# Optimization experiments

Measured on AMD Instinct MI355X. Metric: run time of the kernel, lower is better.

## Reference

```python
import jax, jax.numpy as jnp
import numpy as np

N_QUBITS = 14
QLCU_LAYERS = 2
BATCH = 128
N_PARAMS = 5 * N_QUBITS * QLCU_LAYERS  # 140


def _rx(t):
    # RX(theta) = [[cos(t/2), -i sin(t/2)], [-i sin(t/2), cos(t/2)]], batched over B -> [B,2,2]
    c = jnp.cos(t * 0.5).astype(jnp.complex64)
    s = (-1j * jnp.sin(t * 0.5)).astype(jnp.complex64)
    return jnp.stack([jnp.stack([c, s], -1), jnp.stack([s, c], -1)], -2)


def _ry(t):
    c = jnp.cos(t * 0.5)
    s = jnp.sin(t * 0.5)
    m = jnp.stack([jnp.stack([c, -s], -1), jnp.stack([s, c], -1)], -2)
    return m.astype(jnp.complex64)


def _rz(t):
    e = jnp.exp(-0.5j * t.astype(jnp.complex64))
    z = jnp.zeros_like(e)
    return jnp.stack([jnp.stack([e, z], -1), jnp.stack([z, jnp.conj(e)], -1)], -2)


def _apply_1q(state, gate, w):
    # state: [B] + [2]*n (wire 0 = most significant axis, PennyLane convention); gate: [B,2,2]
    s = jnp.moveaxis(state, w + 1, 1)
    s = jnp.einsum('bij,bj...->bi...', gate, s)
    return jnp.moveaxis(s, 1, w + 1)


def _apply_crx(state, theta, c, t):
    # controlled-RX: apply RX(theta) on target wire t in the control==1 subspace
    gate = _rx(theta)
    st = jnp.moveaxis(state, c + 1, 1)
    s0, s1 = st[:, 0], st[:, 1]
    ta = t if t > c else t + 1  # target axis inside s1 (control axis removed)
    s1 = jnp.moveaxis(s1, ta, 1)
    s1 = jnp.einsum('bij,bj...->bi...', gate, s1)
    s1 = jnp.moveaxis(s1, 1, ta)
    st = jnp.stack([s0, s1], axis=1)
    return jnp.moveaxis(st, 1, c + 1)


def _circuit(params):
    B = params.shape[0]
    n = N_QUBITS
    state = jnp.zeros((B,) + (2,) * n, jnp.complex64)
    state = state.at[(slice(None),) + (0,) * n].set(1.0)  # |0...0>
    idx = 0
    for _ in range(QLCU_LAYERS):
        for i in range(n):
            state = _apply_1q(state, _rx(params[:, idx]), i)
            state = _apply_1q(state, _ry(params[:, idx + 1]), i)
            state = _apply_1q(state, _rz(params[:, idx + 2]), i)
            idx += 3
        for i in range(n):
            state = _apply_crx(state, params[:, idx], i, (i + 1) % n)
            idx += 1
        for i in range(n - 1, -1, -1):
            state = _apply_crx(state, params[:, idx], i, (i - 1) % n)
            idx += 1
    return state.reshape(B, 2 ** n)


def setup_inputs() -> dict:
    key = jax.random.key(0)
    params = jax.random.normal(key, (BATCH, N_PARAMS), dtype=jnp.float32)
    return {"params": params}


def reference(params):
    # Returns the batched quantum state vector [B, 2**n_qubits] (complex64),
    # matching qml.state() wire ordering (wire 0 = MSB).
    return _circuit(params)
```

## Files before the change

kernel.cpp:

```cpp
#include <hip/hip_runtime.h>
#include <math.h>

constexpr int NQ      = 14;
constexpr int NSTATE  = 1 << 14;
constexpr int NF4     = NSTATE / 2;
constexpr int NPARAMS = 140;
constexpr int BATCH   = 128;
constexpr int THREADS = 1024;

__device__ __forceinline__ unsigned int f2bf(float f) {
    union { float f; unsigned int u; } v; v.f = f;
    return (v.u + 0x7FFFu + ((v.u >> 16) & 1u)) >> 16;
}
__device__ __forceinline__ int SWZ4(int f) { return f ^ ((f >> 3) & 7); }

__device__ __forceinline__ void u_half2(float& ax, float& ay, float& bx, float& by,
                                        float ur, float ui, float vr, float vi) {
    float a0x = ax, a0y = ay, a1x = bx, a1y = by;
    ax =  ur*a0x - ui*a0y + vr*a1x - vi*a1y;
    ay =  ur*a0y + ui*a0x + vr*a1y + vi*a1x;
    bx = -vr*a0x - vi*a0y + ur*a1x + ui*a1y;
    by = -vr*a0y + vi*a0x + ur*a1y - ui*a1x;
}
__device__ __forceinline__ void crx_half(float& ax, float& ay, float& bx, float& by,
                                         float cr, float sr) {
    float a0x = ax, a0y = ay, a1x = bx, a1y = by;
    ax = cr*a0x + sr*a1y;  ay = cr*a0y - sr*a1x;
    bx = cr*a1x + sr*a0y;  by = cr*a1y - sr*a0x;
}

struct G  { int type, pb, c, t; };
struct P2 { int nb, b0, b1, b2, ng; G g0, g1, g2; };

constexpr P2 PS[18] = {
    {3,13,12,11, 3, {0,0,0,13},  {0,3,0,12},  {0,6,0,11}},
    {3,10,9,8,   3, {0,9,0,10},  {0,12,0,9},  {0,15,0,8}},
    {3,7,6,5,    3, {0,18,0,7},  {0,21,0,6},  {0,24,0,5}},
    {3,4,3,2,    3, {0,27,0,4},  {0,30,0,3},  {0,33,0,2}},
    {1,1,0,0,    2, {0,36,0,1},  {0,39,0,0},  {0,0,0,0}},
    {3,13,12,11, 2, {1,42,13,12},{1,43,12,11},{0,0,0,0}},
    {3,11,10,9,  2, {1,44,11,10},{1,45,10,9}, {0,0,0,0}},
    {3,9,8,7,    2, {1,46,9,8},  {1,47,8,7},  {0,0,0,0}},
    {3,7,6,5,    2, {1,48,7,6},  {1,49,6,5},  {0,0,0,0}},
    {3,5,4,3,    2, {1,50,5,4},  {1,51,4,3},  {0,0,0,0}},
    {3,3,2,1,    3, {1,52,3,2},  {1,53,2,1},  {1,54,1,0}},
    {3,13,2,1,   3, {1,55,0,13}, {1,56,0,1},  {1,57,1,2}},
    {3,4,3,2,    2, {1,58,2,3},  {1,59,3,4},  {0,0,0,0}},
    {3,6,5,4,    2, {1,60,4,5},  {1,61,5,6},  {0,0,0,0}},
    {3,8,7,6,    2, {1,62,6,7},  {1,63,7,8},  {0,0,0,0}},
    {3,10,9,8,   2, {1,64,8,9},  {1,65,9,10}, {0,0,0,0}},
    {3,12,11,10, 2, {1,66,10,11},{1,67,11,12},{0,0,0,0}},
    {2,13,12,0,  2, {1,68,12,13},{1,69,13,0}, {0,0,0,0}},
};

struct Sorted { int v[3]; };
constexpr Sorted sort3(int a, int b, int c) {
    Sorted s{{a, b, c}};
    for (int i = 0; i < 3; ++i)
        for (int j = 0; j < 2; ++j)
            if (s.v[j] > s.v[j+1]) { int t = s.v[j]; s.v[j] = s.v[j+1]; s.v[j+1] = t; }
    return s;
}
constexpr int off4(int m, int nb, int b0, int b1, int b2) {
    const int B[3] = { b0 - 1, b1 - 1, b2 - 1 };
    int off = 0;
    for (int j = 0; j < nb; ++j) off |= ((m >> (nb-1-j)) & 1) << B[j];
    return off;
}
constexpr int locbit(int b, int b0, int b1, int b2, int nb) {
    return (b == b0) ? (1 << (nb-1)) : (b == b1) ? (1 << (nb-2)) : (1 << (nb-3));
}
constexpr int touch_mask(P2 ps) {
    const int VN = 1 << ps.nb;
    const G gs[3] = { ps.g0, ps.g1, ps.g2 };
    int t = 0;
    for (int gi = 0; gi < ps.ng; ++gi) {
        G g = gs[gi];
        if (g.type == 0 || g.c == 0) { t = (1 << VN) - 1; break; }
        int cb = locbit(g.c, ps.b0, ps.b1, ps.b2, ps.nb);
        for (int m = 0; m < VN; ++m) if (m & cb) t |= 1 << m;
    }
    return t;
}

template<int PI, int GI, int VN>
__device__ __forceinline__ void apply_g(float4 (&v)[VN], const float2* gcs, int L) {
    constexpr P2 ps = PS[PI];
    constexpr G  g  = (GI == 0) ? ps.g0 : (GI == 1) ? ps.g1 : ps.g2;
    const int pb = L + g.pb;
    if constexpr (g.type == 0) {
        const float2 X = gcs[pb], Y = gcs[pb+1], Z = gcs[pb+2];
        const float cx = X.x, sx = X.y, cy = Y.x, sy = Y.y, cz = Z.x, sz = Z.y;
        const float m0r = cy*cx, m0i = sy*sx, m1r = -sy*cx, m1i = -cy*sx;
        const float ur = cz*m0r + sz*m0i, ui = cz*m0i - sz*m0r;
        const float vr = cz*m1r + sz*m1i, vi = cz*m1i - sz*m1r;
        if constexpr (g.t == 0) {
            #pragma unroll
            for (int m = 0; m < VN; ++m)
                u_half2(v[m].x, v[m].y, v[m].z, v[m].w, ur, ui, vr, vi);
        } else {
            constexpr int tb = locbit(g.t, ps.b0, ps.b1, ps.b2, ps.nb);
            #pragma unroll
            for (int m = 0; m < VN; ++m) {
                if (m & tb) continue;
                u_half2(v[m].x, v[m].y, v[m|tb].x, v[m|tb].y, ur, ui, vr, vi);
                u_half2(v[m].z, v[m].w, v[m|tb].z, v[m|tb].w, ur, ui, vr, vi);
            }
        }
    } else {
        const float2 C = gcs[pb];
        const float cr = C.x, sr = C.y;
        if constexpr (g.c == 0) {
            constexpr int tb = locbit(g.t, ps.b0, ps.b1, ps.b2, ps.nb);
            #pragma unroll
            for (int m = 0; m < VN; ++m) {
                if (m & tb) continue;
                crx_half(v[m].z, v[m].w, v[m|tb].z, v[m|tb].w, cr, sr);
            }
        } else if constexpr (g.t == 0) {
            constexpr int cb = locbit(g.c, ps.b0, ps.b1, ps.b2, ps.nb);
            #pragma unroll
            for (int m = 0; m < VN; ++m) {
                if (!(m & cb)) continue;
                crx_half(v[m].x, v[m].y, v[m].z, v[m].w, cr, sr);
            }
        } else {
            constexpr int cb = locbit(g.c, ps.b0, ps.b1, ps.b2, ps.nb);
            constexpr int tb = locbit(g.t, ps.b0, ps.b1, ps.b2, ps.nb);
            #pragma unroll
            for (int m = 0; m < VN; ++m) {
                if (!(m & cb) || (m & tb)) continue;
                crx_half(v[m].x, v[m].y, v[m|tb].x, v[m|tb].y, cr, sr);
                crx_half(v[m].z, v[m].w, v[m|tb].z, v[m|tb].w, cr, sr);
            }
        }
    }
}

template<int PI>
__device__ __forceinline__ void do_pass(float4* st4, const float2* gcs, int tid, int L) {
    constexpr P2 ps = PS[PI];
    constexpr int NB  = ps.nb;
    constexpr int VN  = 1 << NB;
    constexpr int GPT = 8 >> NB;
    constexpr int TM  = touch_mask(ps);
    constexpr Sorted S = sort3(ps.b0 - 1, (NB > 1 ? ps.b1 - 1 : 99), (NB > 2 ? ps.b2 - 1 : 99));

    #pragma unroll
    for (int h = 0; h < GPT; ++h) {
        int base = tid + (h << 10);
        #pragma unroll
        for (int j = 0; j < NB; ++j) {
            const int m = (1 << S.v[j]) - 1;
            base = ((base & ~m) << 1) | (base & m);
        }
        float4 v[VN];
        #pragma unroll
        for (int m = 0; m < VN; ++m) {
            if (!((TM >> m) & 1)) continue;
            v[m] = st4[SWZ4(base | off4(m, NB, ps.b0, ps.b1, ps.b2))];
        }

        apply_g<PI, 0, VN>(v, gcs, L);
        if constexpr (ps.ng > 1) apply_g<PI, 1, VN>(v, gcs, L);
        if constexpr (ps.ng > 2) apply_g<PI, 2, VN>(v, gcs, L);

        #pragma unroll
        for (int m = 0; m < VN; ++m) {
            if (!((TM >> m) & 1)) continue;
            st4[SWZ4(base | off4(m, NB, ps.b0, ps.b1, ps.b2))] = v[m];
        }
        __builtin_amdgcn_sched_barrier(0);
    }
}

template<int PI>
struct RunPasses {
    static __device__ __forceinline__ void go(float4* st4, const float2* gcs, int tid, int L) {
        __syncthreads();
        do_pass<PI>(st4, gcs, tid, L);
        RunPasses<PI + 1>::go(st4, gcs, tid, L);
    }
};
template<> struct RunPasses<18> {
    static __device__ __forceinline__ void go(float4*, const float2*, int, int) {}
};

__global__ __launch_bounds__(THREADS)
void qsim_kernel(const float* __restrict__ params,
                 unsigned int* __restrict__ out_u32) {
    __shared__ float4 st4[NF4];
    __shared__ float2 gcs[NPARAMS];

    const int b   = blockIdx.x;
    const int tid = threadIdx.x;

    if (tid < NPARAMS) {
        float s, c;
        sincosf(0.5f * params[b * NPARAMS + tid], &s, &c);
        gcs[tid] = make_float2(c, s);
    }
    for (int k = tid; k < NF4; k += THREADS)
        st4[k] = make_float4(k == 0 ? 1.f : 0.f, 0.f, 0.f, 0.f);

    #pragma unroll 1
    for (int layer = 0; layer < 2; ++layer)
        RunPasses<0>::go(st4, gcs, tid, layer * 70);
    __syncthreads();

    uint2* ob = (uint2*)(out_u32 + (size_t)b * NSTATE);
    #pragma unroll
    for (int j = 0; j < 8; ++j) {
        const int f = tid + j * 1024;
        const float4 F = st4[SWZ4(f)];
        uint2 w;
        w.x = f2bf(F.y) | (f2bf(F.x) << 16);
        w.y = f2bf(F.w) | (f2bf(F.z) << 16);
        ob[f] = w;
    }
}

extern "C" void kernel_launch(void* const* d_in, const int* in_sizes, int n_in,
                              void* d_out, int out_size, void* d_ws, size_t ws_size,
                              hipStream_t stream) {
    const float* params = (const float*)d_in[0];
    unsigned int* out = (unsigned int*)d_out;
    qsim_kernel<<<BATCH, THREADS, 0, stream>>>(params, out);
}
```

Measured before the change: 60.32 us.

## Regroup gate passes to fuse single-qubit and CRX gates across both layers

Replaces the per-layer 18-pass schedule, run twice in a loop, with one fully unrolled 31-pass schedule. Each pass now carries up to seven gates, so the rotation gates on a qubit triple are fused with the following CRX gates, and the last CRX of layer one is merged with the first rotations of layer two. This lowers the total number of shared-memory sweeps and the barriers between them. It also adds cheap 2-bit passes and pins the VGPR budget at 128. Fully unrolling both layers increases code size, and the register cap could cause spills.

```diff
diff --git a/kernel.cpp b/kernel.cpp
--- a/kernel.cpp
+++ b/kernel.cpp
@@ -30,27 +30,41 @@
 }
 
 struct G  { int type, pb, c, t; };
-struct P2 { int nb, b0, b1, b2, ng; G g0, g1, g2; };
-
-constexpr P2 PS[18] = {
-    {3,13,12,11, 3, {0,0,0,13},  {0,3,0,12},  {0,6,0,11}},
-    {3,10,9,8,   3, {0,9,0,10},  {0,12,0,9},  {0,15,0,8}},
-    {3,7,6,5,    3, {0,18,0,7},  {0,21,0,6},  {0,24,0,5}},
-    {3,4,3,2,    3, {0,27,0,4},  {0,30,0,3},  {0,33,0,2}},
-    {1,1,0,0,    2, {0,36,0,1},  {0,39,0,0},  {0,0,0,0}},
-    {3,13,12,11, 2, {1,42,13,12},{1,43,12,11},{0,0,0,0}},
-    {3,11,10,9,  2, {1,44,11,10},{1,45,10,9}, {0,0,0,0}},
-    {3,9,8,7,    2, {1,46,9,8},  {1,47,8,7},  {0,0,0,0}},
-    {3,7,6,5,    2, {1,48,7,6},  {1,49,6,5},  {0,0,0,0}},
-    {3,5,4,3,    2, {1,50,5,4},  {1,51,4,3},  {0,0,0,0}},
-    {3,3,2,1,    3, {1,52,3,2},  {1,53,2,1},  {1,54,1,0}},
-    {3,13,2,1,   3, {1,55,0,13}, {1,56,0,1},  {1,57,1,2}},
-    {3,4,3,2,    2, {1,58,2,3},  {1,59,3,4},  {0,0,0,0}},
-    {3,6,5,4,    2, {1,60,4,5},  {1,61,5,6},  {0,0,0,0}},
-    {3,8,7,6,    2, {1,62,6,7},  {1,63,7,8},  {0,0,0,0}},
-    {3,10,9,8,   2, {1,64,8,9},  {1,65,9,10}, {0,0,0,0}},
-    {3,12,11,10, 2, {1,66,10,11},{1,67,11,12},{0,0,0,0}},
-    {2,13,12,0,  2, {1,68,12,13},{1,69,13,0}, {0,0,0,0}},
+struct P2 { int nb, b0, b1, b2, ng; G g[7]; };
+
+constexpr P2 PS[31] = {
+    {3,13,12,11, 5, {{0,0,0,13},{0,3,0,12},{0,6,0,11},{1,42,13,12},{1,43,12,11}}},
+    {2,11,10,0,  2, {{0,9,0,10},{1,44,11,10}}},
+    {3,10,9,8,   4, {{0,12,0,9},{0,15,0,8},{1,45,10,9},{1,46,9,8}}},
+    {2,8,7,0,    2, {{0,18,0,7},{1,47,8,7}}},
+    {3,7,6,5,    4, {{0,21,0,6},{0,24,0,5},{1,48,7,6},{1,49,6,5}}},
+    {2,5,4,0,    2, {{0,27,0,4},{1,50,5,4}}},
+    {3,4,3,2,    4, {{0,30,0,3},{0,33,0,2},{1,51,4,3},{1,52,3,2}}},
+    {2,2,1,0,    2, {{0,36,0,1},{1,53,2,1}}},
+    {1,1,0,0,    2, {{0,39,0,0},{1,54,1,0}}},
+    {3,13,2,1,   3, {{1,55,0,13},{1,56,0,1},{1,57,1,2}}},
+    {3,4,3,2,    2, {{1,58,2,3},{1,59,3,4}}},
+    {3,6,5,4,    2, {{1,60,4,5},{1,61,5,6}}},
+    {3,8,7,6,    2, {{1,62,6,7},{1,63,7,8}}},
+    {3,10,9,8,   2, {{1,64,8,9},{1,65,9,10}}},
+    {3,12,11,10, 2, {{1,66,10,11},{1,67,11,12}}},
+    {3,13,12,11, 7, {{1,68,12,13},{1,69,13,0},{0,70,0,13},{0,73,0,12},{0,76,0,11},
+                     {1,112,13,12},{1,113,12,11}}},
+    {2,11,10,0,  2, {{0,79,0,10},{1,114,11,10}}},
+    {3,10,9,8,   4, {{0,82,0,9},{0,85,0,8},{1,115,10,9},{1,116,9,8}}},
+    {2,8,7,0,    2, {{0,88,0,7},{1,117,8,7}}},
+    {3,7,6,5,    4, {{0,91,0,6},{0,94,0,5},{1,118,7,6},{1,119,6,5}}},
+    {2,5,4,0,    2, {{0,97,0,4},{1,120,5,4}}},
+    {3,4,3,2,    4, {{0,100,0,3},{0,103,0,2},{1,121,4,3},{1,122,3,2}}},
+    {2,2,1,0,    2, {{0,106,0,1},{1,123,2,1}}},
+    {1,1,0,0,    2, {{0,109,0,0},{1,124,1,0}}},
+    {3,13,2,1,   3, {{1,125,0,13},{1,126,0,1},{1,127,1,2}}},
+    {3,4,3,2,    2, {{1,128,2,3},{1,129,3,4}}},
+    {3,6,5,4,    2, {{1,130,4,5},{1,131,5,6}}},
+    {3,8,7,6,    2, {{1,132,6,7},{1,133,7,8}}},
+    {3,10,9,8,   2, {{1,134,8,9},{1,135,9,10}}},
+    {3,12,11,10, 2, {{1,136,10,11},{1,137,11,12}}},
+    {2,13,12,0,  2, {{1,138,12,13},{1,139,13,0}}},
 };
 
 struct Sorted { int v[3]; };
@@ -72,10 +86,9 @@
 }
 constexpr int touch_mask(P2 ps) {
     const int VN = 1 << ps.nb;
-    const G gs[3] = { ps.g0, ps.g1, ps.g2 };
     int t = 0;
     for (int gi = 0; gi < ps.ng; ++gi) {
-        G g = gs[gi];
+        G g = ps.g[gi];
         if (g.type == 0 || g.c == 0) { t = (1 << VN) - 1; break; }
         int cb = locbit(g.c, ps.b0, ps.b1, ps.b2, ps.nb);
         for (int m = 0; m < VN; ++m) if (m & cb) t |= 1 << m;
@@ -84,12 +97,11 @@
 }
 
 template<int PI, int GI, int VN>
-__device__ __forceinline__ void apply_g(float4 (&v)[VN], const float2* gcs, int L) {
+__device__ __forceinline__ void apply_g(float4 (&v)[VN], const float2* gcs) {
     constexpr P2 ps = PS[PI];
-    constexpr G  g  = (GI == 0) ? ps.g0 : (GI == 1) ? ps.g1 : ps.g2;
-    const int pb = L + g.pb;
+    constexpr G  g  = ps.g[GI];
     if constexpr (g.type == 0) {
-        const float2 X = gcs[pb], Y = gcs[pb+1], Z = gcs[pb+2];
+        const float2 X = gcs[g.pb], Y = gcs[g.pb+1], Z = gcs[g.pb+2];
         const float cx = X.x, sx = X.y, cy = Y.x, sy = Y.y, cz = Z.x, sz = Z.y;
         const float m0r = cy*cx, m0i = sy*sx, m1r = -sy*cx, m1i = -cy*sx;
         const float ur = cz*m0r + sz*m0i, ui = cz*m0i - sz*m0r;
@@ -108,7 +120,7 @@
             }
         }
     } else {
-        const float2 C = gcs[pb];
+        const float2 C = gcs[g.pb];
         const float cr = C.x, sr = C.y;
         if constexpr (g.c == 0) {
             constexpr int tb = locbit(g.t, ps.b0, ps.b1, ps.b2, ps.nb);
@@ -137,8 +149,16 @@
     }
 }
 
+template<int PI, int GI, int VN>
+__device__ __forceinline__ void apply_chain(float4 (&v)[VN], const float2* gcs) {
+    if constexpr (GI < PS[PI].ng) {
+        apply_g<PI, GI, VN>(v, gcs);
+        apply_chain<PI, GI + 1, VN>(v, gcs);
+    }
+}
+
 template<int PI>
-__device__ __forceinline__ void do_pass(float4* st4, const float2* gcs, int tid, int L) {
+__device__ __forceinline__ void do_pass(float4* st4, const float2* gcs, int tid) {
     constexpr P2 ps = PS[PI];
     constexpr int NB  = ps.nb;
     constexpr int VN  = 1 << NB;
@@ -161,9 +181,7 @@
             v[m] = st4[SWZ4(base | off4(m, NB, ps.b0, ps.b1, ps.b2))];
         }
 
-        apply_g<PI, 0, VN>(v, gcs, L);
-        if constexpr (ps.ng > 1) apply_g<PI, 1, VN>(v, gcs, L);
-        if constexpr (ps.ng > 2) apply_g<PI, 2, VN>(v, gcs, L);
+        apply_chain<PI, 0, VN>(v, gcs);
 
         #pragma unroll
         for (int m = 0; m < VN; ++m) {
@@ -176,17 +194,19 @@
 
 template<int PI>
 struct RunPasses {
-    static __device__ __forceinline__ void go(float4* st4, const float2* gcs, int tid, int L) {
+    static __device__ __forceinline__ void go(float4* st4, const float2* gcs, int tid) {
         __syncthreads();
-        do_pass<PI>(st4, gcs, tid, L);
-        RunPasses<PI + 1>::go(st4, gcs, tid, L);
+        do_pass<PI>(st4, gcs, tid);
+        RunPasses<PI + 1>::go(st4, gcs, tid);
     }
 };
-template<> struct RunPasses<18> {
-    static __device__ __forceinline__ void go(float4*, const float2*, int, int) {}
+template<> struct RunPasses<31> {
+    static __device__ __forceinline__ void go(float4*, const float2*, int) {}
 };
 
-__global__ __launch_bounds__(THREADS)
+__global__
+__attribute__((amdgpu_flat_work_group_size(1024, 1024)))
+__attribute__((amdgpu_num_vgpr(128)))
 void qsim_kernel(const float* __restrict__ params,
                  unsigned int* __restrict__ out_u32) {
     __shared__ float4 st4[NF4];
@@ -203,9 +223,7 @@
     for (int k = tid; k < NF4; k += THREADS)
         st4[k] = make_float4(k == 0 ? 1.f : 0.f, 0.f, 0.f, 0.f);
 
-    #pragma unroll 1
-    for (int layer = 0; layer < 2; ++layer)
-        RunPasses<0>::go(st4, gcs, tid, layer * 70);
+    RunPasses<0>::go(st4, gcs, tid);
     __syncthreads();
 
     uint2* ob = (uint2*)(out_u32 + (size_t)b * NSTATE);
```

Measured after the change: 54.47 us. 1.11x faster.
